# Kernel tuning notes

Measured on AMD Instinct MI355X. Metric: run time of the kernel, lower is better.

The kernel has to match this reference:

```python
import jax, jax.numpy as jnp
import numpy as np

E = 65536      # num edges
T = 262144     # num triplets
H = 128        # hidden_channels
D = 64         # int_emb_size
C = 8          # basis_emb_size
NR = 6         # num_radial
NS = 7         # num_spherical
NB = 6         # len(bt_list) = num_BT + 1
BT_LIST = (-1, 0, 1, 2, 3, 4)
NBS = 1        # num_before_skip (also used for after-skip list in original code)


def setup_inputs() -> dict:
    key = jax.random.key(0)
    ks = iter(jax.random.split(key, 40))
    s = 0.05
    p = lambda shape: jax.random.normal(next(ks), shape, dtype=jnp.float32) * s
    inp = dict(
        x=jax.random.normal(next(ks), (E, H), dtype=jnp.float32),
        rbf=jax.random.normal(next(ks), (E, NR), dtype=jnp.float32),
        sbf=jax.random.normal(next(ks), (T, NS * NR), dtype=jnp.float32),
        idx_kj=jax.random.randint(next(ks), (T,), 0, E),
        idx_ji=jax.random.randint(next(ks), (T,), 0, E),
        bt=jax.random.randint(next(ks), (E,), 0, 5),
        lambda_d=1,
        alpha=jnp.float32(0.7),
        # per-branch stacked weights (6 branches)
        W_kj=p((NB, H, H)), b_kj=jnp.zeros((NB, H), jnp.float32),
        W_rbf1=p((NB, NR, C)), W_rbf2=p((NB, C, H)),
        W_sbf1=p((NB, NS * NR, C)), W_sbf2=p((NB, C, D)),
        W_down=p((NB, H, D)),
        W_ji=p((H, H)), b_ji=jnp.zeros((H,), jnp.float32),
        W_up=p((D, H)),
        rb1_w=p((NBS, H, H)), rb1_b=jnp.zeros((NBS, H), jnp.float32),
        rb2_w=p((NBS, H, H)), rb2_b=jnp.zeros((NBS, H), jnp.float32),
        W_lin=p((H, H)), b_lin=jnp.zeros((H,), jnp.float32),
        ra1_w=p((NBS, H, H)), ra1_b=jnp.zeros((NBS, H), jnp.float32),
        ra2_w=p((NBS, H, H)), ra2_b=jnp.zeros((NBS, H), jnp.float32),
    )
    return inp


def reference(x, rbf, sbf, idx_kj, idx_ji, bt, lambda_d, alpha,
              W_kj, b_kj, W_rbf1, W_rbf2, W_sbf1, W_sbf2, W_down,
              W_ji, b_ji, W_up, rb1_w, rb1_b, rb2_w, rb2_b,
              W_lin, b_lin, ra1_w, ra1_b, ra2_w, ra2_b):
    act = jax.nn.silu

    x_ji = act(x @ W_ji + b_ji)                                  # [E,H]

    # per-branch edge transforms, vectorized over the 6 branches (axis b)
    tmp = act(jnp.einsum('eh,bhg->beg', x, W_kj) + b_kj[:, None, :])   # [B,E,H]
    rbf_p = jnp.einsum('er,brc->bec', rbf, W_rbf1)                     # [B,E,C]
    rbf_p = jnp.einsum('bec,bcg->beg', rbf_p, W_rbf2)                  # [B,E,H]
    tmp = tmp * rbf_p
    down = act(jnp.einsum('beh,bhd->bed', tmp, W_down))                # [B,E,D]

    sbf_p = jnp.einsum('ts,bsc->btc', sbf, W_sbf1)                     # [B,T,C]
    sbf_p = jnp.einsum('btc,bcd->btd', sbf_p, W_sbf2)                  # [B,T,D]

    spe = down[:, idx_kj, :] * sbf_p                                   # [B,T,D]

    # last branch scattered with weight alpha
    x_kj_tot = alpha * jax.ops.segment_sum(spe[-1], idx_ji, num_segments=E)

    # per band-type masked scatter with weight (1 - alpha)
    bt_trip = bt[idx_kj]                                               # [T]
    for b, btv in enumerate(BT_LIST):
        m = (bt_trip == btv).astype(x.dtype)[:, None]
        x_kj_tot = x_kj_tot + (1.0 - alpha) * jax.ops.segment_sum(
            spe[b] * m, idx_ji, num_segments=E)

    x_kj = act(x_kj_tot @ W_up)                                        # [E,H]
    h = x_ji + x_kj
    for i in range(rb1_w.shape[0]):
        h = h + act(act(h @ rb1_w[i] + rb1_b[i]) @ rb2_w[i] + rb2_b[i])
    h = act(h @ W_lin + b_lin) + x
    for i in range(ra1_w.shape[0]):
        h = h + act(act(h @ ra1_w[i] + ra1_b[i]) @ ra2_w[i] + ra2_b[i])
    return h
```

## Files before the change

kernel.cpp:

```cpp
#include <hip/hip_runtime.h>
#include <hip/hip_bf16.h>
#include <stdint.h>

typedef __bf16 bf16_t;
typedef bf16_t bf16x8 __attribute__((ext_vector_type(8)));
typedef bf16_t bf16x2 __attribute__((ext_vector_type(2)));
typedef float f32x4 __attribute__((ext_vector_type(4)));

#define E_N 65536
#define T_N 262144

__device__ __forceinline__ float silu_f(float v) {
  return v / (1.0f + __expf(-v));
}

__device__ __forceinline__ int permrow(int n) {
  return (n & ~31) | ((n & 1) << 4) | ((n & 30) >> 1);
}

__device__ __forceinline__ uint32_t pack_bf16(float a, float b) {
  union { bf16x2 h; uint32_t u; } u;
  u.h[0] = (bf16_t)a; u.h[1] = (bf16_t)b;
  return u.u;
}

__device__ __forceinline__ float2 ubf2f(uint32_t v) {
  union { uint32_t u; bf16x2 h; } c; c.u = v;
  return make_float2((float)c.h[0], (float)c.h[1]);
}

__device__ __forceinline__ void atomic_pk_add_bf16(bf16_t* addr, uint32_t val) {
  asm volatile("global_atomic_pk_add_bf16 %0, %1, off" :: "v"(addr), "v"(val) : "memory");
}

template<int KI, int NTJ, int BS>
__device__ __forceinline__ void gemm_bg(const bf16_t* A, const bf16_t* __restrict__ Bg,
                                        int mb, int nb, int l16, int q,
                                        f32x4 (&acc)[2][NTJ]) {
  bf16x8 bfr[KI][NTJ];
  const bf16_t* bp = Bg + (nb + l16) * BS + q * 8;
#pragma unroll
  for (int kt = 0; kt < KI; ++kt)
#pragma unroll
    for (int tj = 0; tj < NTJ; ++tj)
      bfr[kt][tj] = *(const bf16x8*)(bp + tj * 16 * BS + kt * 32);
#pragma unroll
  for (int kt = 0; kt < KI; ++kt) {
    const int sw = ((kt * 4 + q) ^ l16) << 3;
    bf16x8 a0 = *(const bf16x8*)(A + ((mb + l16) << 7) + sw);
    bf16x8 a1 = *(const bf16x8*)(A + ((mb + 16 + l16) << 7) + sw);
#pragma unroll
    for (int tj = 0; tj < NTJ; ++tj) {
      acc[0][tj] = __builtin_amdgcn_mfma_f32_16x16x32_bf16(a0, bfr[kt][tj], acc[0][tj], 0, 0, 0);
      acc[1][tj] = __builtin_amdgcn_mfma_f32_16x16x32_bf16(a1, bfr[kt][tj], acc[1][tj], 0, 0, 0);
    }
  }
}

template<int C4>
__device__ __forceinline__ void stage_x(bf16_t* dst, const float* src, int tid) {
  const float4* g = (const float4*)src;
#pragma unroll
  for (int i = tid; i < 64 * C4; i += 256) {
    const int row = i / C4, c4 = i % C4;
    float4 v = g[i];
    bf16_t t[4] = {(bf16_t)v.x, (bf16_t)v.y, (bf16_t)v.z, (bf16_t)v.w};
    *(uint2*)(dst + (row << 7) + ((((c4 >> 1) ^ (row & 15)) << 3) | ((c4 & 1) << 2))) =
        *(const uint2*)t;
  }
}

__device__ __forceinline__ void stage_xkj(bf16_t* dst, const bf16_t* src, int tid) {
  const uint4* g = (const uint4*)src;
#pragma unroll
  for (int i = tid; i < 64 * 8; i += 256) {
    const int row = i >> 3, k8 = i & 7;
    *(uint4*)(dst + (row << 7) + ((k8 ^ (row & 15)) << 3)) = g[i];
  }
}

__global__ void prep_kernel(
    const float* __restrict__ W_ji, const float* __restrict__ W_kj,
    const float* __restrict__ W_down, const float* __restrict__ W_up,
    const float* __restrict__ rb1, const float* __restrict__ rb2,
    const float* __restrict__ W_lin, const float* __restrict__ ra1,
    const float* __restrict__ ra2, const float* __restrict__ W_rbf1,
    const float* __restrict__ W_rbf2, const float* __restrict__ W_sbf1,
    const float* __restrict__ W_sbf2,
    bf16_t* __restrict__ wjiT, bf16_t* __restrict__ wkjT,
    bf16_t* __restrict__ wdownT, bf16_t* __restrict__ wupT,
    bf16_t* __restrict__ rb1T, bf16_t* __restrict__ rb2T,
    bf16_t* __restrict__ linT, bf16_t* __restrict__ ra1T,
    bf16_t* __restrict__ ra2T, bf16_t* __restrict__ wcb,
    bf16_t* __restrict__ wsT)
{
  const int tid = threadIdx.x;
  const int bx = blockIdx.x;
  if (bx < 112) {
    const int c = bx * 256 + tid;
    const float* src; bf16_t* dst; int n, k8, N, K;
    if (c < 22528) {
      const int m = c >> 11, w = c & 2047;
      n = w >> 4; k8 = w & 15; N = 128; K = 128;
      if (m == 0)      { src = W_ji;  dst = wjiT; }
      else if (m <= 5) { src = W_kj + m * 16384; dst = wkjT + (m - 1) * 16384; }
      else if (m == 6) { src = rb1;   dst = rb1T; }
      else if (m == 7) { src = rb2;   dst = rb2T; }
      else if (m == 8) { src = W_lin; dst = linT; }
      else if (m == 9) { src = ra1;   dst = ra1T; }
      else             { src = ra2;   dst = ra2T; }
    } else if (c < 27648) {
      const int m = (c - 22528) >> 10, w = (c - 22528) & 1023;
      n = w >> 4; k8 = w & 15; N = 64; K = 128;
      src = W_down + (m + 1) * 8192; dst = wdownT + m * 8192;
    } else {
      const int w = c - 27648;
      n = w >> 3; k8 = w & 7; N = 128; K = 64;
      src = W_up; dst = wupT;
    }
    bf16_t t[8];
#pragma unroll
    for (int j = 0; j < 8; ++j) t[j] = (bf16_t)src[(k8 * 8 + j) * N + n];
    *(uint4*)(dst + permrow(n) * K + k8 * 8) = *(const uint4*)t;
  } else if (bx < 115) {
    const int o = (bx - 112) * 256 + tid;
    if (o < 640) {
      const int slot = o >> 7, n = o & 127;
      const int b = slot + 1;
      bf16_t t[32];
#pragma unroll
      for (int k = 0; k < 32; ++k) t[k] = (bf16_t)0.f;
#pragma unroll
      for (int r = 0; r < 6; ++r) {
        float s = 0.f;
#pragma unroll
        for (int c = 0; c < 8; ++c)
          s += W_rbf1[b * 48 + r * 8 + c] * W_rbf2[b * 1024 + c * 128 + n];
        t[r] = (bf16_t)s;
      }
      bf16_t* dst = wcb + slot * 4096 + permrow(n) * 32;
#pragma unroll
      for (int g = 0; g < 4; ++g) *(uint4*)(dst + g * 8) = *(const uint4*)(t + g * 8);
    }
  } else {
    const int o = (bx - 115) * 256 + tid;
    if (o < 320) {
      const int slot = o >> 6, j = o & 63;
      const int b = slot + 1;
      bf16_t t[64];
#pragma unroll
      for (int s = 0; s < 64; ++s) {
        float v = 0.f;
        if (s < 42) {
#pragma unroll
          for (int c = 0; c < 8; ++c)
            v += W_sbf1[b * 336 + s * 8 + c] * W_sbf2[b * 512 + c * 64 + j];
        }
        t[s] = (bf16_t)v;
      }
      bf16_t* dst = wsT + (slot * 64 + permrow(j)) * 64;
#pragma unroll
      for (int g = 0; g < 8; ++g) *(uint4*)(dst + g * 8) = *(const uint4*)(t + g * 8);
    }
  }
}

__global__ __launch_bounds__(256, 3)
void edge_kernel(const float* __restrict__ x, const float* __restrict__ rbf,
                 const float* __restrict__ b_kj, const float* __restrict__ b_ji,
                 const bf16_t* __restrict__ wjiT, const bf16_t* __restrict__ wkjT,
                 const bf16_t* __restrict__ wdownT, const bf16_t* __restrict__ wcb,
                 bf16_t* __restrict__ x_ji_out, bf16_t* __restrict__ down)
{
  __shared__ bf16_t xA[64 * 128];
  __shared__ bf16_t tmpA[64 * 128];
  __shared__ bf16_t rbfA[64 * 32];
  __shared__ float biasS[128];

  const int tid = threadIdx.x;
  const int lane = tid & 63, wv = tid >> 6;
  const int q = lane >> 4, l16 = lane & 15;
  const int mb = (wv >> 1) * 32, nb = (wv & 1) * 64;
  const int R = blockIdx.x * 64;
  const int br = blockIdx.y;

  stage_x<32>(xA, x + (size_t)R * 128, tid);
  if (tid < 128) biasS[tid] = (br == 0) ? b_ji[tid] : b_kj[br * 128 + tid];
  if (br != 0 && tid < 64) {
    const float* rg = rbf + (size_t)(R + tid) * 6;
    bf16_t t[8] = {(bf16_t)rg[0], (bf16_t)rg[1], (bf16_t)rg[2],
                   (bf16_t)rg[3], (bf16_t)rg[4], (bf16_t)rg[5],
                   (bf16_t)0.f, (bf16_t)0.f};
    const uint4 z = {0, 0, 0, 0};
    bf16_t* dst = rbfA + tid * 32;
#pragma unroll
    for (int g = 0; g < 4; ++g) *(uint4*)(dst + g * 8) = z;
    *(uint4*)(dst + ((tid & 3) << 3)) = *(const uint4*)t;
  }
  __syncthreads();

  const bf16_t* WB = (br == 0) ? wjiT : wkjT + (size_t)(br - 1) * 16384;
  f32x4 acc[2][4] = {};
  gemm_bg<4, 4, 128>(xA, WB, mb, nb, l16, q, acc);

  if (br == 0) {
#pragma unroll
    for (int ti = 0; ti < 2; ++ti)
#pragma unroll
      for (int r = 0; r < 4; ++r) {
        const int row = mb + ti * 16 + q * 4 + r;
#pragma unroll
        for (int gl = 0; gl < 2; ++gl) {
          const int col0 = nb + gl * 32 + 2 * l16;
          const float2 b2 = *(const float2*)&biasS[col0];
          *(uint32_t*)&x_ji_out[(size_t)(R + row) * 128 + col0] =
              pack_bf16(silu_f(acc[ti][2 * gl][r] + b2.x),
                        silu_f(acc[ti][2 * gl + 1][r] + b2.y));
        }
      }
    return;
  }

  f32x4 accr[2][4] = {};
  {
    const int sw = (q ^ (l16 & 3)) << 3;
    bf16x8 a0 = *(const bf16x8*)(rbfA + ((mb + l16) << 5) + sw);
    bf16x8 a1 = *(const bf16x8*)(rbfA + ((mb + 16 + l16) << 5) + sw);
    const bf16_t* wb = wcb + (size_t)(br - 1) * 4096 + (nb + l16) * 32 + q * 8;
    bf16x8 bf0 = *(const bf16x8*)(wb);
    bf16x8 bf1 = *(const bf16x8*)(wb + 16 * 32);
    bf16x8 bf2 = *(const bf16x8*)(wb + 32 * 32);
    bf16x8 bf3 = *(const bf16x8*)(wb + 48 * 32);
    accr[0][0] = __builtin_amdgcn_mfma_f32_16x16x32_bf16(a0, bf0, accr[0][0], 0, 0, 0);
    accr[1][0] = __builtin_amdgcn_mfma_f32_16x16x32_bf16(a1, bf0, accr[1][0], 0, 0, 0);
    accr[0][1] = __builtin_amdgcn_mfma_f32_16x16x32_bf16(a0, bf1, accr[0][1], 0, 0, 0);
    accr[1][1] = __builtin_amdgcn_mfma_f32_16x16x32_bf16(a1, bf1, accr[1][1], 0, 0, 0);
    accr[0][2] = __builtin_amdgcn_mfma_f32_16x16x32_bf16(a0, bf2, accr[0][2], 0, 0, 0);
    accr[1][2] = __builtin_amdgcn_mfma_f32_16x16x32_bf16(a1, bf2, accr[1][2], 0, 0, 0);
    accr[0][3] = __builtin_amdgcn_mfma_f32_16x16x32_bf16(a0, bf3, accr[0][3], 0, 0, 0);
    accr[1][3] = __builtin_amdgcn_mfma_f32_16x16x32_bf16(a1, bf3, accr[1][3], 0, 0, 0);
  }

#pragma unroll
  for (int ti = 0; ti < 2; ++ti)
#pragma unroll
    for (int r = 0; r < 4; ++r) {
      const int row = mb + ti * 16 + q * 4 + r;
#pragma unroll
      for (int gl = 0; gl < 2; ++gl) {
        const int col0 = nb + gl * 32 + 2 * l16;
        const float2 b2 = *(const float2*)&biasS[col0];
        const float v0 = silu_f(acc[ti][2 * gl][r] + b2.x) * accr[ti][2 * gl][r];
        const float v1 = silu_f(acc[ti][2 * gl + 1][r] + b2.y) * accr[ti][2 * gl + 1][r];
        *(uint32_t*)&tmpA[(row << 7) + ((((col0 >> 3) ^ (row & 15)) << 3) | (col0 & 7))] =
            pack_bf16(v0, v1);
      }
    }
  __syncthreads();

  const int nb2 = (wv & 1) * 32;
  f32x4 acc2[2][2] = {};
  gemm_bg<4, 2, 128>(tmpA, wdownT + (size_t)(br - 1) * 8192, mb, nb2, l16, q, acc2);
#pragma unroll
  for (int ti = 0; ti < 2; ++ti)
#pragma unroll
    for (int r = 0; r < 4; ++r) {
      const int row = mb + ti * 16 + q * 4 + r;
      const int col0 = nb2 + 2 * l16;
      *(uint32_t*)&down[((size_t)(R + row) * 5 + (br - 1)) * 64 + col0] =
          pack_bf16(silu_f(acc2[ti][0][r]), silu_f(acc2[ti][1][r]));
    }
}

__global__ __launch_bounds__(256, 3)
void triplet_kernel(const float* __restrict__ sbf, const int* __restrict__ idx_kj,
                    const int* __restrict__ idx_ji, const int* __restrict__ bt,
                    const float* __restrict__ alpha_p, const bf16_t* __restrict__ wsT,
                    const bf16_t* __restrict__ down, bf16_t* __restrict__ xkj)
{
  __shared__ bf16_t s_sbf[64 * 64];
  __shared__ bf16_t spC[64 * 344];
  __shared__ int s_kj[64], s_ji[64], s_bs[64];

  const int tid = threadIdx.x;
  const int lane = tid & 63, wv = tid >> 6;
  const int q = lane >> 4, l16 = lane & 15;
  const int base = blockIdx.x * 64;

  if (tid < 64) {
    const int kj = idx_kj[base + tid];
    s_kj[tid] = kj;
    s_ji[tid] = idx_ji[base + tid];
    s_bs[tid] = bt[kj];
  }
#pragma unroll
  for (int it = 0; it < 2; ++it) {
    const int i = tid + it * 256;
    const int row = i >> 3, k8 = i & 7;
    const float* sg = sbf + (size_t)(base + row) * 42 + k8 * 8;
    bf16_t t[8];
#pragma unroll
    for (int jj = 0; jj < 8; ++jj)
      t[jj] = (k8 * 8 + jj < 42) ? (bf16_t)sg[jj] : (bf16_t)0.f;
    *(uint4*)(s_sbf + (row << 6) + ((k8 ^ (row & 7)) << 3)) = *(const uint4*)t;
  }
  __syncthreads();

  const int mb = (wv & 1) * 32;
  const int tb0 = (wv >> 1) * 10;
  f32x4 acc[2][10] = {};
#pragma unroll
  for (int kt = 0; kt < 2; ++kt) {
    const int sw = (((kt << 2) + q) ^ (l16 & 7)) << 3;
    bf16x8 a0 = *(const bf16x8*)(s_sbf + ((mb + l16) << 6) + sw);
    bf16x8 a1 = *(const bf16x8*)(s_sbf + ((mb + 16 + l16) << 6) + sw);
    const bf16_t* bp = wsT + (tb0 * 16 + l16) * 64 + (kt << 5) + (q << 3);
#pragma unroll
    for (int tj = 0; tj < 10; ++tj) {
      bf16x8 b = *(const bf16x8*)(bp + tj * 1024);
      acc[0][tj] = __builtin_amdgcn_mfma_f32_16x16x32_bf16(a0, b, acc[0][tj], 0, 0, 0);
      acc[1][tj] = __builtin_amdgcn_mfma_f32_16x16x32_bf16(a1, b, acc[1][tj], 0, 0, 0);
    }
  }
#pragma unroll
  for (int ti = 0; ti < 2; ++ti)
#pragma unroll
    for (int r = 0; r < 4; ++r) {
      const int row = mb + ti * 16 + q * 4 + r;
#pragma unroll
      for (int tp = 0; tp < 5; ++tp) {
        const int t0 = tb0 + 2 * tp;
        const int col = (t0 >> 2) * 64 + (((t0 & 3) >> 1) << 5) + 2 * l16;
        *(uint32_t*)&spC[row * 344 + col] =
            pack_bf16(acc[ti][2 * tp][r], acc[ti][2 * tp + 1][r]);
      }
    }
  __syncthreads();

  const float alpha = alpha_p[0];
  const float oma = 1.f - alpha;
  const int hf = lane >> 5;
  const int j0 = (lane & 31) * 2;

  uint32_t G5[8], GB[8];
#pragma unroll
  for (int ii = 0; ii < 8; ++ii) {
    const int t = wv * 16 + ii * 2 + hf;
    const bf16_t* dr = down + (size_t)s_kj[t] * 320;
    G5[ii] = *(const uint32_t*)(dr + 256 + j0);
    GB[ii] = *(const uint32_t*)(dr + s_bs[t] * 64 + j0);
  }
#pragma unroll
  for (int ii = 0; ii < 8; ++ii) {
    const int t = wv * 16 + ii * 2 + hf;
    const int slot = s_bs[t];
    const int ji = s_ji[t];
    const float2 d5 = ubf2f(*(const uint32_t*)&spC[t * 344 + 256 + j0]);
    const float2 db = ubf2f(*(const uint32_t*)&spC[t * 344 + slot * 64 + j0]);
    const float2 g5 = ubf2f(G5[ii]);
    const float2 gb = ubf2f(GB[ii]);
    const float r0 = alpha * g5.x * d5.x + oma * gb.x * db.x;
    const float r1 = alpha * g5.y * d5.y + oma * gb.y * db.y;
    atomic_pk_add_bf16(&xkj[(size_t)ji * 64 + j0], pack_bf16(r0, r1));
  }
}

__global__ __launch_bounds__(256, 3)
void epi_kernel(const float* __restrict__ x, const bf16_t* __restrict__ x_ji,
                const bf16_t* __restrict__ xkj,
                const bf16_t* __restrict__ wupT,
                const bf16_t* __restrict__ rb1T, const float* __restrict__ rb1_b,
                const bf16_t* __restrict__ rb2T, const float* __restrict__ rb2_b,
                const bf16_t* __restrict__ linT, const float* __restrict__ lin_b,
                const bf16_t* __restrict__ ra1T, const float* __restrict__ ra1_b,
                const bf16_t* __restrict__ ra2T, const float* __restrict__ ra2_b,
                float* __restrict__ out)
{
  __shared__ bf16_t bufA[64 * 128];
  __shared__ bf16_t bufB[64 * 128];
  __shared__ float biasAll[5 * 128];

  const int tid = threadIdx.x;
  const int lane = tid & 63, wv = tid >> 6;
  const int q = lane >> 4, l16 = lane & 15;
  const int mb = (wv >> 1) * 32, nb = (wv & 1) * 64;
  const int R = blockIdx.x * 64;

  stage_xkj(bufA, xkj + (size_t)R * 64, tid);
  if (tid < 128) {
    biasAll[tid]       = rb1_b[tid];
    biasAll[128 + tid] = rb2_b[tid];
    biasAll[256 + tid] = lin_b[tid];
    biasAll[384 + tid] = ra1_b[tid];
    biasAll[512 + tid] = ra2_b[tid];
  }
  __syncthreads();

  f32x4 hreg[2][4];
  {
    f32x4 acc[2][4] = {};
    gemm_bg<2, 4, 64>(bufA, wupT, mb, nb, l16, q, acc);
#pragma unroll
    for (int ti = 0; ti < 2; ++ti)
#pragma unroll
      for (int r = 0; r < 4; ++r) {
        const int row = mb + ti * 16 + q * 4 + r;
#pragma unroll
        for (int gl = 0; gl < 2; ++gl) {
          const int col0 = nb + gl * 32 + 2 * l16;
          union { uint32_t u; bf16x2 h; } xj;
          xj.u = *(const uint32_t*)&x_ji[(size_t)(R + row) * 128 + col0];
          const float h0 = (float)xj.h[0] + silu_f(acc[ti][2 * gl][r]);
          const float h1 = (float)xj.h[1] + silu_f(acc[ti][2 * gl + 1][r]);
          hreg[ti][2 * gl][r] = h0;
          hreg[ti][2 * gl + 1][r] = h1;
          *(uint32_t*)&bufB[(row << 7) + ((((col0 >> 3) ^ (row & 15)) << 3) | (col0 & 7))] =
              pack_bf16(h0, h1);
        }
      }
  }

#define EPI_STAGE(ASRC, WPTR, BROW, BODY)                                        \
  __syncthreads();                                                               \
  {                                                                              \
    f32x4 acc[2][4] = {};                                                        \
    gemm_bg<4, 4, 128>(ASRC, WPTR, mb, nb, l16, q, acc);                         \
    _Pragma("unroll")                                                            \
    for (int ti = 0; ti < 2; ++ti)                                               \
      _Pragma("unroll")                                                          \
      for (int r = 0; r < 4; ++r) {                                              \
        const int row = mb + ti * 16 + q * 4 + r;                                \
        _Pragma("unroll")                                                        \
        for (int gl = 0; gl < 2; ++gl) {                                         \
          const int col0 = nb + gl * 32 + 2 * l16;                               \
          const float2 b2 = *(const float2*)&biasAll[BROW * 128 + col0];         \
          const float g0 = acc[ti][2 * gl][r] + b2.x;                            \
          const float g1 = acc[ti][2 * gl + 1][r] + b2.y;                        \
          BODY                                                                   \
        }                                                                        \
      }                                                                          \
  }

  EPI_STAGE(bufB, rb1T, 0, {
    *(uint32_t*)&bufA[(row << 7) + ((((col0 >> 3) ^ (row & 15)) << 3) | (col0 & 7))] =
        pack_bf16(silu_f(g0), silu_f(g1));
  })

  EPI_STAGE(bufA, rb2T, 1, {
    const float h0 = hreg[ti][2 * gl][r] + silu_f(g0);
    const float h1 = hreg[ti][2 * gl + 1][r] + silu_f(g1);
    hreg[ti][2 * gl][r] = h0; hreg[ti][2 * gl + 1][r] = h1;
    *(uint32_t*)&bufB[(row << 7) + ((((col0 >> 3) ^ (row & 15)) << 3) | (col0 & 7))] =
        pack_bf16(h0, h1);
  })

  EPI_STAGE(bufB, linT, 2, {
    const float2 xv = *(const float2*)&x[(size_t)(R + row) * 128 + col0];
    const float h0 = silu_f(g0) + xv.x;
    const float h1 = silu_f(g1) + xv.y;
    hreg[ti][2 * gl][r] = h0; hreg[ti][2 * gl + 1][r] = h1;
    *(uint32_t*)&bufA[(row << 7) + ((((col0 >> 3) ^ (row & 15)) << 3) | (col0 & 7))] =
        pack_bf16(h0, h1);
  })

  EPI_STAGE(bufA, ra1T, 3, {
    *(uint32_t*)&bufB[(row << 7) + ((((col0 >> 3) ^ (row & 15)) << 3) | (col0 & 7))] =
        pack_bf16(silu_f(g0), silu_f(g1));
  })

  EPI_STAGE(bufB, ra2T, 4, {
    float2 o;
    o.x = hreg[ti][2 * gl][r] + silu_f(g0);
    o.y = hreg[ti][2 * gl + 1][r] + silu_f(g1);
    *(float2*)&out[(size_t)(R + row) * 128 + col0] = o;
  })
#undef EPI_STAGE
}

extern "C" void kernel_launch(void* const* d_in, const int* in_sizes, int n_in,
                              void* d_out, int out_size, void* d_ws, size_t ws_size,
                              hipStream_t stream)
{
  (void)in_sizes; (void)n_in; (void)out_size; (void)ws_size;
  const float* x      = (const float*)d_in[0];
  const float* rbf    = (const float*)d_in[1];
  const float* sbf    = (const float*)d_in[2];
  const int*   idx_kj = (const int*)d_in[3];
  const int*   idx_ji = (const int*)d_in[4];
  const int*   bt     = (const int*)d_in[5];
  const float* alpha  = (const float*)d_in[7];
  const float* W_kj   = (const float*)d_in[8];
  const float* b_kj   = (const float*)d_in[9];
  const float* W_rbf1 = (const float*)d_in[10];
  const float* W_rbf2 = (const float*)d_in[11];
  const float* W_sbf1 = (const float*)d_in[12];
  const float* W_sbf2 = (const float*)d_in[13];
  const float* W_down = (const float*)d_in[14];
  const float* W_ji   = (const float*)d_in[15];
  const float* b_ji   = (const float*)d_in[16];
  const float* W_up   = (const float*)d_in[17];
  const float* rb1_w  = (const float*)d_in[18];
  const float* rb1_b  = (const float*)d_in[19];
  const float* rb2_w  = (const float*)d_in[20];
  const float* rb2_b  = (const float*)d_in[21];
  const float* W_lin  = (const float*)d_in[22];
  const float* b_lin  = (const float*)d_in[23];
  const float* ra1_w  = (const float*)d_in[24];
  const float* ra1_b  = (const float*)d_in[25];
  const float* ra2_w  = (const float*)d_in[26];
  const float* ra2_b  = (const float*)d_in[27];

  char* ws = (char*)d_ws;
  bf16_t* down   = (bf16_t*)(ws);
  bf16_t* x_ji   = (bf16_t*)(ws + 41943040);
  bf16_t* xkj    = (bf16_t*)(ws + 58720256);
  char* wbase    = ws + 75497472;
  bf16_t* wjiT   = (bf16_t*)(wbase + 0);
  bf16_t* wkjT   = (bf16_t*)(wbase + 32768);
  bf16_t* wdownT = (bf16_t*)(wbase + 196608);
  bf16_t* wupT   = (bf16_t*)(wbase + 278528);
  bf16_t* rb1T   = (bf16_t*)(wbase + 294912);
  bf16_t* rb2T   = (bf16_t*)(wbase + 327680);
  bf16_t* linT   = (bf16_t*)(wbase + 360448);
  bf16_t* ra1T   = (bf16_t*)(wbase + 393216);
  bf16_t* ra2T   = (bf16_t*)(wbase + 425984);
  bf16_t* wcb    = (bf16_t*)(wbase + 458752);
  bf16_t* wsT    = (bf16_t*)(wbase + 499712);

  hipMemsetAsync(xkj, 0, (size_t)E_N * 64 * 2, stream);
  prep_kernel<<<117, 256, 0, stream>>>(W_ji, W_kj, W_down, W_up, rb1_w, rb2_w,
                                       W_lin, ra1_w, ra2_w, W_rbf1, W_rbf2,
                                       W_sbf1, W_sbf2,
                                       wjiT, wkjT, wdownT, wupT, rb1T, rb2T,
                                       linT, ra1T, ra2T, wcb, wsT);
  edge_kernel<<<dim3(E_N / 64, 6), 256, 0, stream>>>(x, rbf, b_kj, b_ji, wjiT,
                                                     wkjT, wdownT, wcb, x_ji, down);
  triplet_kernel<<<T_N / 64, 256, 0, stream>>>(sbf, idx_kj, idx_ji, bt, alpha,
                                               wsT, down, xkj);
  epi_kernel<<<E_N / 64, 256, 0, stream>>>(x, x_ji, xkj, wupT, rb1T, rb1_b,
                                           rb2T, rb2_b, linT, b_lin,
                                           ra1T, ra1_b, ra2T, ra2_b,
                                           (float*)d_out);
}
```

Before: 392.5 us.

## Replace atomic scatter with bucketed gather, register-stage x, widen epilogue blocks

The triplet kernel no longer scatters into xkj with bf16 atomics. It writes per-triplet contributions to a buffer, and a new fill kernel buckets triplets by idx_ji (up to 12 per edge, extras go to an overflow list). A gather kernel then sums each edge's bucket, and an overflow kernel handles the rest with atomics. Separately, edge_kernel loads x straight into MFMA A-fragments in registers instead of staging through LDS, and epi_kernel moves to 512 threads with 32-column tiles per wave. The gather removes atomic contention but adds an extra 32MB write and read of contributions plus an extra kernel, and the triplet-to-edge summation order is now nondeterministic.

```diff
diff --git a/kernel.cpp b/kernel.cpp
--- a/kernel.cpp
+++ b/kernel.cpp
@@ -31,6 +31,13 @@
 
 __device__ __forceinline__ void atomic_pk_add_bf16(bf16_t* addr, uint32_t val) {
   asm volatile("global_atomic_pk_add_bf16 %0, %1, off" :: "v"(addr), "v"(val) : "memory");
+}
+
+__device__ __forceinline__ bf16x8 pack8(float4 a, float4 b) {
+  union { bf16x8 v; uint32_t u[4]; } z;
+  z.u[0] = pack_bf16(a.x, a.y); z.u[1] = pack_bf16(a.z, a.w);
+  z.u[2] = pack_bf16(b.x, b.y); z.u[3] = pack_bf16(b.z, b.w);
+  return z.v;
 }
 
 template<int KI, int NTJ, int BS>
@@ -57,25 +64,28 @@
   }
 }
 
-template<int C4>
-__device__ __forceinline__ void stage_x(bf16_t* dst, const float* src, int tid) {
-  const float4* g = (const float4*)src;
-#pragma unroll
-  for (int i = tid; i < 64 * C4; i += 256) {
-    const int row = i / C4, c4 = i % C4;
-    float4 v = g[i];
-    bf16_t t[4] = {(bf16_t)v.x, (bf16_t)v.y, (bf16_t)v.z, (bf16_t)v.w};
-    *(uint2*)(dst + (row << 7) + ((((c4 >> 1) ^ (row & 15)) << 3) | ((c4 & 1) << 2))) =
-        *(const uint2*)t;
-  }
-}
-
-__device__ __forceinline__ void stage_xkj(bf16_t* dst, const bf16_t* src, int tid) {
-  const uint4* g = (const uint4*)src;
-#pragma unroll
-  for (int i = tid; i < 64 * 8; i += 256) {
-    const int row = i >> 3, k8 = i & 7;
-    *(uint4*)(dst + (row << 7) + ((k8 ^ (row & 15)) << 3)) = g[i];
+template<int KI, int NTJ, int BS>
+__device__ __forceinline__ void gemm_rg(const bf16x8 (&a0)[KI], const bf16x8 (&a1)[KI],
+                                        const bf16_t* __restrict__ Bg,
+                                        int nb, int l16, int q, f32x4 (&acc)[2][NTJ]) {
+  const bf16_t* bp = Bg + (nb + l16) * BS + q * 8;
+  bf16x8 bcur[NTJ], bnxt[NTJ];
+#pragma unroll
+  for (int tj = 0; tj < NTJ; ++tj) bcur[tj] = *(const bf16x8*)(bp + tj * 16 * BS);
+#pragma unroll
+  for (int kt = 0; kt < KI; ++kt) {
+    if (kt + 1 < KI) {
+#pragma unroll
+      for (int tj = 0; tj < NTJ; ++tj)
+        bnxt[tj] = *(const bf16x8*)(bp + tj * 16 * BS + (kt + 1) * 32);
+    }
+#pragma unroll
+    for (int tj = 0; tj < NTJ; ++tj) {
+      acc[0][tj] = __builtin_amdgcn_mfma_f32_16x16x32_bf16(a0[kt], bcur[tj], acc[0][tj], 0, 0, 0);
+      acc[1][tj] = __builtin_amdgcn_mfma_f32_16x16x32_bf16(a1[kt], bcur[tj], acc[1][tj], 0, 0, 0);
+    }
+#pragma unroll
+    for (int tj = 0; tj < NTJ; ++tj) bcur[tj] = bnxt[tj];
   }
 }
 
@@ -165,14 +175,27 @@
   }
 }
 
-__global__ __launch_bounds__(256, 3)
+__global__ void fill_kernel(const int* __restrict__ idx_ji, int* __restrict__ cnt,
+                            int* __restrict__ bucket, int* __restrict__ ovfc,
+                            int* __restrict__ ovf)
+{
+  const int t = blockIdx.x * 256 + threadIdx.x;
+  const int ji = idx_ji[t];
+  const int pos = atomicAdd(&cnt[ji], 1);
+  if (pos < 12) bucket[ji * 12 + pos] = t;
+  else {
+    const int o = atomicAdd(ovfc, 1);
+    if (o < 65536) ovf[o] = t;
+  }
+}
+
+__global__ __launch_bounds__(256, 4)
 void edge_kernel(const float* __restrict__ x, const float* __restrict__ rbf,
                  const float* __restrict__ b_kj, const float* __restrict__ b_ji,
                  const bf16_t* __restrict__ wjiT, const bf16_t* __restrict__ wkjT,
                  const bf16_t* __restrict__ wdownT, const bf16_t* __restrict__ wcb,
                  bf16_t* __restrict__ x_ji_out, bf16_t* __restrict__ down)
 {
-  __shared__ bf16_t xA[64 * 128];
   __shared__ bf16_t tmpA[64 * 128];
   __shared__ bf16_t rbfA[64 * 32];
   __shared__ float biasS[128];
@@ -184,7 +207,6 @@
   const int R = blockIdx.x * 64;
   const int br = blockIdx.y;
 
-  stage_x<32>(xA, x + (size_t)R * 128, tid);
   if (tid < 128) biasS[tid] = (br == 0) ? b_ji[tid] : b_kj[br * 128 + tid];
   if (br != 0 && tid < 64) {
     const float* rg = rbf + (size_t)(R + tid) * 6;
@@ -197,11 +219,25 @@
     for (int g = 0; g < 4; ++g) *(uint4*)(dst + g * 8) = z;
     *(uint4*)(dst + ((tid & 3) << 3)) = *(const uint4*)t;
   }
+
+  bf16x8 af0[4], af1[4];
+  {
+    const float* xr = x + (size_t)(R + mb + l16) * 128 + q * 8;
+#pragma unroll
+    for (int kt = 0; kt < 4; ++kt) {
+      float4 v0 = *(const float4*)(xr + kt * 32);
+      float4 v1 = *(const float4*)(xr + kt * 32 + 4);
+      float4 w0 = *(const float4*)(xr + 16 * 128 + kt * 32);
+      float4 w1 = *(const float4*)(xr + 16 * 128 + kt * 32 + 4);
+      af0[kt] = pack8(v0, v1);
+      af1[kt] = pack8(w0, w1);
+    }
+  }
   __syncthreads();
 
   const bf16_t* WB = (br == 0) ? wjiT : wkjT + (size_t)(br - 1) * 16384;
   f32x4 acc[2][4] = {};
-  gemm_bg<4, 4, 128>(xA, WB, mb, nb, l16, q, acc);
+  gemm_rg<4, 4, 128>(af0, af1, WB, nb, l16, q, acc);
 
   if (br == 0) {
 #pragma unroll
@@ -227,18 +263,12 @@
     bf16x8 a0 = *(const bf16x8*)(rbfA + ((mb + l16) << 5) + sw);
     bf16x8 a1 = *(const bf16x8*)(rbfA + ((mb + 16 + l16) << 5) + sw);
     const bf16_t* wb = wcb + (size_t)(br - 1) * 4096 + (nb + l16) * 32 + q * 8;
-    bf16x8 bf0 = *(const bf16x8*)(wb);
-    bf16x8 bf1 = *(const bf16x8*)(wb + 16 * 32);
-    bf16x8 bf2 = *(const bf16x8*)(wb + 32 * 32);
-    bf16x8 bf3 = *(const bf16x8*)(wb + 48 * 32);
-    accr[0][0] = __builtin_amdgcn_mfma_f32_16x16x32_bf16(a0, bf0, accr[0][0], 0, 0, 0);
-    accr[1][0] = __builtin_amdgcn_mfma_f32_16x16x32_bf16(a1, bf0, accr[1][0], 0, 0, 0);
-    accr[0][1] = __builtin_amdgcn_mfma_f32_16x16x32_bf16(a0, bf1, accr[0][1], 0, 0, 0);
-    accr[1][1] = __builtin_amdgcn_mfma_f32_16x16x32_bf16(a1, bf1, accr[1][1], 0, 0, 0);
-    accr[0][2] = __builtin_amdgcn_mfma_f32_16x16x32_bf16(a0, bf2, accr[0][2], 0, 0, 0);
-    accr[1][2] = __builtin_amdgcn_mfma_f32_16x16x32_bf16(a1, bf2, accr[1][2], 0, 0, 0);
-    accr[0][3] = __builtin_amdgcn_mfma_f32_16x16x32_bf16(a0, bf3, accr[0][3], 0, 0, 0);
-    accr[1][3] = __builtin_amdgcn_mfma_f32_16x16x32_bf16(a1, bf3, accr[1][3], 0, 0, 0);
+#pragma unroll
+    for (int tj = 0; tj < 4; ++tj) {
+      bf16x8 b = *(const bf16x8*)(wb + tj * 16 * 32);
+      accr[0][tj] = __builtin_amdgcn_mfma_f32_16x16x32_bf16(a0, b, accr[0][tj], 0, 0, 0);
+      accr[1][tj] = __builtin_amdgcn_mfma_f32_16x16x32_bf16(a1, b, accr[1][tj], 0, 0, 0);
+    }
   }
 
 #pragma unroll
@@ -274,13 +304,13 @@
 
 __global__ __launch_bounds__(256, 3)
 void triplet_kernel(const float* __restrict__ sbf, const int* __restrict__ idx_kj,
-                    const int* __restrict__ idx_ji, const int* __restrict__ bt,
+                    const int* __restrict__ bt,
                     const float* __restrict__ alpha_p, const bf16_t* __restrict__ wsT,
-                    const bf16_t* __restrict__ down, bf16_t* __restrict__ xkj)
+                    const bf16_t* __restrict__ down, bf16_t* __restrict__ contrib)
 {
   __shared__ bf16_t s_sbf[64 * 64];
   __shared__ bf16_t spC[64 * 344];
-  __shared__ int s_kj[64], s_ji[64], s_bs[64];
+  __shared__ int s_kj[64], s_bs[64];
 
   const int tid = threadIdx.x;
   const int lane = tid & 63, wv = tid >> 6;
@@ -290,7 +320,6 @@
   if (tid < 64) {
     const int kj = idx_kj[base + tid];
     s_kj[tid] = kj;
-    s_ji[tid] = idx_ji[base + tid];
     s_bs[tid] = bt[kj];
   }
 #pragma unroll
@@ -354,18 +383,48 @@
   for (int ii = 0; ii < 8; ++ii) {
     const int t = wv * 16 + ii * 2 + hf;
     const int slot = s_bs[t];
-    const int ji = s_ji[t];
     const float2 d5 = ubf2f(*(const uint32_t*)&spC[t * 344 + 256 + j0]);
     const float2 db = ubf2f(*(const uint32_t*)&spC[t * 344 + slot * 64 + j0]);
     const float2 g5 = ubf2f(G5[ii]);
     const float2 gb = ubf2f(GB[ii]);
     const float r0 = alpha * g5.x * d5.x + oma * gb.x * db.x;
     const float r1 = alpha * g5.y * d5.y + oma * gb.y * db.y;
-    atomic_pk_add_bf16(&xkj[(size_t)ji * 64 + j0], pack_bf16(r0, r1));
-  }
-}
-
-__global__ __launch_bounds__(256, 3)
+    *(uint32_t*)&contrib[(size_t)(base + t) * 64 + j0] = pack_bf16(r0, r1);
+  }
+}
+
+__global__ __launch_bounds__(256, 8)
+void gather_kernel(const int* __restrict__ cnt, const int* __restrict__ bucket,
+                   const bf16_t* __restrict__ contrib, bf16_t* __restrict__ xkj)
+{
+  const int wv = threadIdx.x >> 6, lane = threadIdx.x & 63;
+  const int e = blockIdx.x * 4 + wv;
+  int n = cnt[e]; if (n > 12) n = 12;
+  const int tk = (lane < 12) ? bucket[e * 12 + lane] : 0;
+  float acc = 0.f;
+  for (int k = 0; k < n; ++k) {
+    const int t = __shfl(tk, k);
+    acc += (float)contrib[(size_t)t * 64 + lane];
+  }
+  xkj[(size_t)e * 64 + lane] = (bf16_t)acc;
+}
+
+__global__ void ovf_kernel(const int* __restrict__ ovfc, const int* __restrict__ ovf,
+                           const int* __restrict__ idx_ji,
+                           const bf16_t* __restrict__ contrib, bf16_t* __restrict__ xkj)
+{
+  int m = *ovfc; if (m > 65536) m = 65536;
+  const int gid = blockIdx.x * 256 + threadIdx.x;
+  const int entry0 = gid >> 5, pl = gid & 31;
+  for (int i = entry0; i < m; i += (gridDim.x * 256) >> 5) {
+    const int t = ovf[i];
+    const int ji = idx_ji[t];
+    const uint32_t v = *(const uint32_t*)&contrib[(size_t)t * 64 + pl * 2];
+    atomic_pk_add_bf16(&xkj[(size_t)ji * 64 + pl * 2], v);
+  }
+}
+
+__global__ __launch_bounds__(512, 4)
 void epi_kernel(const float* __restrict__ x, const bf16_t* __restrict__ x_ji,
                 const bf16_t* __restrict__ xkj,
                 const bf16_t* __restrict__ wupT,
@@ -383,10 +442,14 @@
   const int tid = threadIdx.x;
   const int lane = tid & 63, wv = tid >> 6;
   const int q = lane >> 4, l16 = lane & 15;
-  const int mb = (wv >> 1) * 32, nb = (wv & 1) * 64;
+  const int mb = (wv >> 2) * 32, nb = (wv & 3) * 32;
   const int R = blockIdx.x * 64;
 
-  stage_xkj(bufA, xkj + (size_t)R * 64, tid);
+  {
+    const int row = tid >> 3, k8 = tid & 7;
+    *(uint4*)(bufA + (row << 7) + ((k8 ^ (row & 15)) << 3)) =
+        ((const uint4*)(xkj + (size_t)R * 64))[tid];
+  }
   if (tid < 128) {
     biasAll[tid]       = rb1_b[tid];
     biasAll[128 + tid] = rb2_b[tid];
@@ -396,48 +459,42 @@
   }
   __syncthreads();
 
-  f32x4 hreg[2][4];
+  f32x4 hreg[2][2];
   {
-    f32x4 acc[2][4] = {};
-    gemm_bg<2, 4, 64>(bufA, wupT, mb, nb, l16, q, acc);
+    f32x4 acc[2][2] = {};
+    gemm_bg<2, 2, 64>(bufA, wupT, mb, nb, l16, q, acc);
 #pragma unroll
     for (int ti = 0; ti < 2; ++ti)
 #pragma unroll
       for (int r = 0; r < 4; ++r) {
         const int row = mb + ti * 16 + q * 4 + r;
-#pragma unroll
-        for (int gl = 0; gl < 2; ++gl) {
-          const int col0 = nb + gl * 32 + 2 * l16;
-          union { uint32_t u; bf16x2 h; } xj;
-          xj.u = *(const uint32_t*)&x_ji[(size_t)(R + row) * 128 + col0];
-          const float h0 = (float)xj.h[0] + silu_f(acc[ti][2 * gl][r]);
-          const float h1 = (float)xj.h[1] + silu_f(acc[ti][2 * gl + 1][r]);
-          hreg[ti][2 * gl][r] = h0;
-          hreg[ti][2 * gl + 1][r] = h1;
-          *(uint32_t*)&bufB[(row << 7) + ((((col0 >> 3) ^ (row & 15)) << 3) | (col0 & 7))] =
-              pack_bf16(h0, h1);
-        }
+        const int col0 = nb + 2 * l16;
+        union { uint32_t u; bf16x2 h; } xj;
+        xj.u = *(const uint32_t*)&x_ji[(size_t)(R + row) * 128 + col0];
+        const float h0 = (float)xj.h[0] + silu_f(acc[ti][0][r]);
+        const float h1 = (float)xj.h[1] + silu_f(acc[ti][1][r]);
+        hreg[ti][0][r] = h0;
+        hreg[ti][1][r] = h1;
+        *(uint32_t*)&bufB[(row << 7) + ((((col0 >> 3) ^ (row & 15)) << 3) | (col0 & 7))] =
+            pack_bf16(h0, h1);
       }
   }
 
 #define EPI_STAGE(ASRC, WPTR, BROW, BODY)                                        \
   __syncthreads();                                                               \
   {                                                                              \
-    f32x4 acc[2][4] = {};                                                        \
-    gemm_bg<4, 4, 128>(ASRC, WPTR, mb, nb, l16, q, acc);                         \
+    f32x4 acc[2][2] = {};                                                        \
+    gemm_bg<4, 2, 128>(ASRC, WPTR, mb, nb, l16, q, acc);                         \
     _Pragma("unroll")                                                            \
     for (int ti = 0; ti < 2; ++ti)                                               \
       _Pragma("unroll")                                                          \
       for (int r = 0; r < 4; ++r) {                                              \
         const int row = mb + ti * 16 + q * 4 + r;                                \
-        _Pragma("unroll")                                                        \
-        for (int gl = 0; gl < 2; ++gl) {                                         \
-          const int col0 = nb + gl * 32 + 2 * l16;                               \
-          const float2 b2 = *(const float2*)&biasAll[BROW * 128 + col0];         \
-          const float g0 = acc[ti][2 * gl][r] + b2.x;                            \
-          const float g1 = acc[ti][2 * gl + 1][r] + b2.y;                        \
-          BODY                                                                   \
-        }                                                                        \
+        const int col0 = nb + 2 * l16;                                           \
+        const float2 b2 = *(const float2*)&biasAll[BROW * 128 + col0];           \
+        const float g0 = acc[ti][0][r] + b2.x;                                   \
+        const float g1 = acc[ti][1][r] + b2.y;                                   \
+        BODY                                                                     \
       }                                                                          \
   }
 
@@ -447,9 +504,9 @@
   })
 
   EPI_STAGE(bufA, rb2T, 1, {
-    const float h0 = hreg[ti][2 * gl][r] + silu_f(g0);
-    const float h1 = hreg[ti][2 * gl + 1][r] + silu_f(g1);
-    hreg[ti][2 * gl][r] = h0; hreg[ti][2 * gl + 1][r] = h1;
+    const float h0 = hreg[ti][0][r] + silu_f(g0);
+    const float h1 = hreg[ti][1][r] + silu_f(g1);
+    hreg[ti][0][r] = h0; hreg[ti][1][r] = h1;
     *(uint32_t*)&bufB[(row << 7) + ((((col0 >> 3) ^ (row & 15)) << 3) | (col0 & 7))] =
         pack_bf16(h0, h1);
   })
@@ -458,7 +515,7 @@
     const float2 xv = *(const float2*)&x[(size_t)(R + row) * 128 + col0];
     const float h0 = silu_f(g0) + xv.x;
     const float h1 = silu_f(g1) + xv.y;
-    hreg[ti][2 * gl][r] = h0; hreg[ti][2 * gl + 1][r] = h1;
+    hreg[ti][0][r] = h0; hreg[ti][1][r] = h1;
     *(uint32_t*)&bufA[(row << 7) + ((((col0 >> 3) ^ (row & 15)) << 3) | (col0 & 7))] =
         pack_bf16(h0, h1);
   })
@@ -470,8 +527,8 @@
 
   EPI_STAGE(bufB, ra2T, 4, {
     float2 o;
-    o.x = hreg[ti][2 * gl][r] + silu_f(g0);
-    o.y = hreg[ti][2 * gl + 1][r] + silu_f(g1);
+    o.x = hreg[ti][0][r] + silu_f(g0);
+    o.y = hreg[ti][1][r] + silu_f(g1);
     *(float2*)&out[(size_t)(R + row) * 128 + col0] = o;
   })
 #undef EPI_STAGE
@@ -511,10 +568,11 @@
   const float* ra2_b  = (const float*)d_in[27];
 
   char* ws = (char*)d_ws;
-  bf16_t* down   = (bf16_t*)(ws);
-  bf16_t* x_ji   = (bf16_t*)(ws + 41943040);
-  bf16_t* xkj    = (bf16_t*)(ws + 58720256);
-  char* wbase    = ws + 75497472;
+  bf16_t* down    = (bf16_t*)(ws);
+  bf16_t* x_ji    = (bf16_t*)(ws + 41943040);
+  bf16_t* xkj     = (bf16_t*)(ws + 58720256);
+  bf16_t* contrib = (bf16_t*)(ws + 67108864);
+  char* wbase     = ws + 100663296;
   bf16_t* wjiT   = (bf16_t*)(wbase + 0);
   bf16_t* wkjT   = (bf16_t*)(wbase + 32768);
   bf16_t* wdownT = (bf16_t*)(wbase + 196608);
@@ -526,18 +584,25 @@
   bf16_t* ra2T   = (bf16_t*)(wbase + 425984);
   bf16_t* wcb    = (bf16_t*)(wbase + 458752);
   bf16_t* wsT    = (bf16_t*)(wbase + 499712);
-
-  hipMemsetAsync(xkj, 0, (size_t)E_N * 64 * 2, stream);
+  int* cnt    = (int*)(wbase + 540672);
+  int* ovfc   = (int*)(wbase + 802816);
+  int* bucket = (int*)(wbase + 803072);
+  int* ovf    = (int*)(wbase + 3948800);
+
+  hipMemsetAsync(cnt, 0, 262400, stream);
   prep_kernel<<<117, 256, 0, stream>>>(W_ji, W_kj, W_down, W_up, rb1_w, rb2_w,
                                        W_lin, ra1_w, ra2_w, W_rbf1, W_rbf2,
                                        W_sbf1, W_sbf2,
                                        wjiT, wkjT, wdownT, wupT, rb1T, rb2T,
                                        linT, ra1T, ra2T, wcb, wsT);
+  fill_kernel<<<T_N / 256, 256, 0, stream>>>(idx_ji, cnt, bucket, ovfc, ovf);
   edge_kernel<<<dim3(E_N / 64, 6), 256, 0, stream>>>(x, rbf, b_kj, b_ji, wjiT,
                                                      wkjT, wdownT, wcb, x_ji, down);
-  triplet_kernel<<<T_N / 64, 256, 0, stream>>>(sbf, idx_kj, idx_ji, bt, alpha,
-                                               wsT, down, xkj);
-  epi_kernel<<<E_N / 64, 256, 0, stream>>>(x, x_ji, xkj, wupT, rb1T, rb1_b,
+  triplet_kernel<<<T_N / 64, 256, 0, stream>>>(sbf, idx_kj, bt, alpha,
+                                               wsT, down, contrib);
+  gather_kernel<<<E_N / 4, 256, 0, stream>>>(cnt, bucket, contrib, xkj);
+  ovf_kernel<<<32, 256, 0, stream>>>(ovfc, ovf, idx_ji, contrib, xkj);
+  epi_kernel<<<E_N / 64, 512, 0, stream>>>(x, x_ji, xkj, wupT, rb1T, rb1_b,
                                            rb2T, rb2_b, linT, b_lin,
                                            ra1T, ra1_b, ra2T, ra2_b,
                                            (float*)d_out);
```

Result: slower. 448.9 us (+14.3%).
